# Kernel tuning notes

Hardware: AMD Instinct MI355X
Metric: run time of the kernel (lower is better)

## Reference

```python
import jax, jax.numpy as jnp
import numpy as np

N = 50000      # nodes
E = 400000     # edges
IN = 256       # in_dim
OUT = 64       # out_dim per head
ED = 64        # edge_dim
H = 4          # num_heads


def setup_inputs() -> dict:
    key = jax.random.key(0)
    ks = jax.random.split(key, 12)
    s = 0.05  # weight scale
    return {
        "x": jax.random.normal(ks[0], (N, IN), jnp.float32),
        "edge_index": jax.random.randint(ks[1], (2, E), 0, N),
        "edge_attr": jax.random.normal(ks[2], (E, ED), jnp.float32),
        # per-head stacked parameters
        "W_fc": jax.random.normal(ks[3], (H, IN, OUT), jnp.float32) * s,
        "b_fc": jnp.zeros((H, OUT), jnp.float32),
        "W_att": jax.random.normal(ks[4], (H, 2 * OUT + ED), jnp.float32) * s,
        "b_att": jnp.zeros((H,), jnp.float32),
        "W_edge": jax.random.normal(ks[5], (H, ED, OUT), jnp.float32) * s,
        "b_edge": jnp.zeros((H, OUT), jnp.float32),
        "W_eatt": jax.random.normal(ks[6], (H, ED, ED), jnp.float32) * s,
        "b_eatt": jnp.zeros((H, ED), jnp.float32),
    }


def reference(x, edge_index, edge_attr, W_fc, b_fc, W_att, b_att,
              W_edge, b_edge, W_eatt, b_eatt):
    src = edge_index[0]  # x_j (source / message sender)
    dst = edge_index[1]  # x_i (destination / aggregation index)

    # node transform per head: z[h] = x @ W_fc[h] + b_fc[h]   -> [H, N, OUT]
    z = jnp.einsum('ni,hio->hno', x, W_fc) + b_fc[:, None, :]
    # edge transform for attention calc: [H, E, ED]
    ea = jnp.einsum('ef,hfg->heg', edge_attr, W_eatt) + b_eatt[:, None, :]
    # edge transform for aggregation: [H, E, OUT]
    ez = jnp.einsum('ef,hfo->heo', edge_attr, W_edge) + b_edge[:, None, :]

    # attn_fc(cat[x_i, x_j, ea]) decomposed: W_att = [Wi | Wj | We]
    Wi = W_att[:, :OUT]            # [H, OUT]
    Wj = W_att[:, OUT:2 * OUT]     # [H, OUT]
    We = W_att[:, 2 * OUT:]        # [H, ED]
    a_node_i = jnp.einsum('hno,ho->hn', z, Wi)  # [H, N]
    a_node_j = jnp.einsum('hno,ho->hn', z, Wj)  # [H, N]
    a = (a_node_i[:, dst] + a_node_j[:, src]
         + jnp.einsum('heg,hg->he', ea, We) + b_att[:, None])  # [H, E]
    e = jax.nn.leaky_relu(a, negative_slope=0.2)

    # segment softmax over destination nodes, per head
    seg_max = jax.vmap(lambda v: jax.ops.segment_max(v, dst, num_segments=N))(e)
    exp_e = jnp.exp(e - seg_max[:, dst])
    seg_sum = jax.vmap(lambda v: jax.ops.segment_sum(v, dst, num_segments=N))(exp_e)
    alpha = exp_e / seg_sum[:, dst]  # [H, E]

    # weighted message: alpha * (x_j + ez), scatter-add to destination
    msg = alpha[:, :, None] * (z[:, src, :] + ez)  # [H, E, OUT]
    out = jax.vmap(lambda m: jax.ops.segment_sum(m, dst, num_segments=N))(msg)  # [H, N, OUT]

    # merge == 'cat' over heads -> [N, H*OUT]
    cat_out = jnp.transpose(out, (1, 0, 2)).reshape(N, H * OUT)
    return cat_out, alpha
```

## Files before the change

### kernel.cpp

```cpp
#include <hip/hip_runtime.h>
#include <math.h>

#define N_NODES 50000
#define N_EDGES 400000
#define IN_F 256
#define OUT_F 64
#define ED_F 64
#define NH 4
#define SCAN_NB ((N_NODES + 255) / 256)

using f16x8 = __attribute__((ext_vector_type(8))) _Float16;
using f32x4 = __attribute__((ext_vector_type(4))) float;

__global__ __launch_bounds__(256) void prep_kernel(
    const float* __restrict__ W_att, const float* __restrict__ b_att,
    const float* __restrict__ W_eatt, const float* __restrict__ b_eatt,
    const float* __restrict__ W_fc, const float* __restrict__ W_edge,
    float* __restrict__ u, float* __restrict__ c,
    _Float16* __restrict__ Wfcfrag, _Float16* __restrict__ Wefrag)
{
    const int b = blockIdx.x, t = threadIdx.x;
    if (b == 0) {
        int h = t >> 6, f = t & 63;
        const float* We = W_att + h * (2 * OUT_F + ED_F) + 2 * OUT_F;
        float s = 0.f;
        for (int g = 0; g < ED_F; g++) s += W_eatt[(h * ED_F + f) * ED_F + g] * We[g];
        u[t] = s;
        if (f == 0) {
            float cc = b_att[h];
            for (int g = 0; g < ED_F; g++) cc += b_eatt[h * ED_F + g] * We[g];
            c[h] = cc;
        }
    } else if (b <= 32) {
        int idx = b - 1;
        int h = idx >> 3, kt = idx & 7;
        int lane = t & 63, nt = t >> 6;
        int q = lane >> 4, l15 = lane & 15;
        f16x8 w;
#pragma unroll
        for (int j = 0; j < 8; j++) {
            int k = kt * 32 + q * 8 + j;
            int o = nt * 16 + l15;
            w[j] = (_Float16)W_fc[((size_t)h * IN_F + k) * OUT_F + o];
        }
        *(f16x8*)&Wfcfrag[(size_t)(((h * 8 + kt) * 4 + nt) * 64 + lane) * 8] = w;
    } else {
        int idx = b - 33;
        int h = idx >> 1, kt = idx & 1;
        int lane = t & 63, nt = t >> 6;
        int q = lane >> 4, l15 = lane & 15;
        f16x8 w;
#pragma unroll
        for (int j = 0; j < 8; j++) {
            int k = kt * 32 + q * 8 + j;
            int o = nt * 16 + l15;
            w[j] = (_Float16)W_edge[((size_t)h * ED_F + k) * OUT_F + o];
        }
        *(f16x8*)&Wefrag[(size_t)(((h * 2 + kt) * 4 + nt) * 64 + lane) * 8] = w;
    }
}

__global__ __launch_bounds__(256) void z_gemm(
    const float* __restrict__ x, const _Float16* __restrict__ Wfcfrag,
    const float* __restrict__ b_fc, const float* __restrict__ W_att,
    _Float16* __restrict__ zb, float* __restrict__ a_i, float* __restrict__ a_j)
{
    __shared__ _Float16 aLDS[32 * 64 * 8];
    const int t = threadIdx.x;
    const int n0 = blockIdx.x * 64;
    const int lane = t & 63, h = t >> 6;
    const int q = lane >> 4, l15 = lane & 15;

    {
        const int m = t >> 2, qq = t & 3;
        const int n = n0 + m;
#pragma unroll
        for (int p = 0; p < 4; p++) {
            float4 v4[4];
            if (n < N_NODES) {
                const float4* xp = (const float4*)(x + (size_t)n * IN_F + p * 64 + qq * 16);
#pragma unroll
                for (int k = 0; k < 4; k++) v4[k] = xp[k];
            } else {
#pragma unroll
                for (int k = 0; k < 4; k++) v4[k] = make_float4(0.f, 0.f, 0.f, 0.f);
            }
            const float* vv = (const float*)v4;
#pragma unroll
            for (int i = 0; i < 2; i++) {
                int c8 = p * 8 + qq * 2 + i;
                f16x8 w;
#pragma unroll
                for (int j = 0; j < 8; j++) w[j] = (_Float16)vv[i * 8 + j];
                *(f16x8*)&aLDS[(c8 * 64 + m) * 8] = w;
            }
        }
    }
    __syncthreads();

    f32x4 acc[4][4];
#pragma unroll
    for (int mt = 0; mt < 4; mt++)
#pragma unroll
        for (int nt = 0; nt < 4; nt++) acc[mt][nt] = (f32x4)0.f;

    for (int kt = 0; kt < 8; kt++) {
        f16x8 bfr[4];
#pragma unroll
        for (int nt = 0; nt < 4; nt++)
            bfr[nt] = *(const f16x8*)&Wfcfrag[(size_t)(((h * 8 + kt) * 4 + nt) * 64 + lane) * 8];
        f16x8 afr[4];
#pragma unroll
        for (int mt = 0; mt < 4; mt++)
            afr[mt] = *(f16x8*)&aLDS[((kt * 4 + q) * 64 + mt * 16 + l15) * 8];
#pragma unroll
        for (int mt = 0; mt < 4; mt++)
#pragma unroll
            for (int nt = 0; nt < 4; nt++)
                acc[mt][nt] = __builtin_amdgcn_mfma_f32_16x16x32_f16(afr[mt], bfr[nt], acc[mt][nt], 0, 0, 0);
    }

    float bfc[4], wiv[4], wjv[4];
#pragma unroll
    for (int nt = 0; nt < 4; nt++) {
        bfc[nt] = b_fc[h * OUT_F + nt * 16 + l15];
        wiv[nt] = W_att[h * 192 + nt * 16 + l15];
        wjv[nt] = W_att[h * 192 + 64 + nt * 16 + l15];
    }

#pragma unroll
    for (int mt = 0; mt < 4; mt++) {
#pragma unroll
        for (int r = 0; r < 4; r++) {
            const int node = n0 + mt * 16 + q * 4 + r;
            float zv[4];
            float pi = 0.f, pj = 0.f;
#pragma unroll
            for (int nt = 0; nt < 4; nt++) {
                zv[nt] = acc[mt][nt][r] + bfc[nt];
                pi += zv[nt] * wiv[nt];
                pj += zv[nt] * wjv[nt];
            }
#pragma unroll
            for (int m = 8; m; m >>= 1) {
                pi += __shfl_xor(pi, m, 64);
                pj += __shfl_xor(pj, m, 64);
            }
            if (node < N_NODES) {
                _Float16* zrow = zb + ((size_t)h * N_NODES + node) * OUT_F;
#pragma unroll
                for (int nt = 0; nt < 4; nt++)
                    zrow[nt * 16 + l15] = (_Float16)zv[nt];
                if (l15 == 0) {
                    a_i[h * N_NODES + node] = pi;
                    a_j[h * N_NODES + node] = pj;
                }
            }
        }
    }
}


__global__ __launch_bounds__(256) void hist_kernel(
    const int* __restrict__ edge_index, int* __restrict__ deg)
{
    const int e = blockIdx.x * 256 + threadIdx.x;
    if (e < N_EDGES) atomicAdd(&deg[edge_index[N_EDGES + e]], 1);
}

__global__ __launch_bounds__(256) void scan1_kernel(
    const int* __restrict__ deg, int* __restrict__ row_ptr, int* __restrict__ bsum)
{
    __shared__ int wsum[4];
    const int t = threadIdx.x, lane = t & 63, w = t >> 6;
    const int idx = blockIdx.x * 256 + t;
    int v = (idx < N_NODES) ? deg[idx] : 0;
    int x = v;
#pragma unroll
    for (int off = 1; off < 64; off <<= 1) {
        int y = __shfl_up(x, off, 64);
        if (lane >= off) x += y;
    }
    if (lane == 63) wsum[w] = x;
    __syncthreads();
    int woff = 0;
#pragma unroll
    for (int i = 0; i < 4; i++) if (i < w) woff += wsum[i];
    if (idx < N_NODES) row_ptr[idx] = woff + x - v;
    if (t == 255) bsum[blockIdx.x] = woff + x;
}

__global__ __launch_bounds__(256) void scan2_kernel(int* __restrict__ bsum)
{
    __shared__ int wsum[4];
    const int t = threadIdx.x, lane = t & 63, w = t >> 6;
    int v = (t < SCAN_NB) ? bsum[t] : 0;
    int x = v;
#pragma unroll
    for (int off = 1; off < 64; off <<= 1) {
        int y = __shfl_up(x, off, 64);
        if (lane >= off) x += y;
    }
    if (lane == 63) wsum[w] = x;
    __syncthreads();
    int woff = 0;
#pragma unroll
    for (int i = 0; i < 4; i++) if (i < w) woff += wsum[i];
    __syncthreads();
    if (t < SCAN_NB) bsum[t] = woff + x - v;
}

__global__ __launch_bounds__(256) void scan3_kernel(
    const int* __restrict__ bsum, int* __restrict__ row_ptr, int* __restrict__ cursor)
{
    const int idx = blockIdx.x * 256 + threadIdx.x;
    if (idx < N_NODES) {
        int rp = row_ptr[idx] + bsum[blockIdx.x];
        row_ptr[idx] = rp;
        cursor[idx] = rp;
    } else if (idx == N_NODES) {
        row_ptr[N_NODES] = N_EDGES;
    }
}

__global__ __launch_bounds__(256) void scatter_kernel(
    const int* __restrict__ edge_index, int* __restrict__ cursor,
    int* __restrict__ eorig, int* __restrict__ ssrc, int* __restrict__ sdst)
{
    const int e = blockIdx.x * 256 + threadIdx.x;
    if (e >= N_EDGES) return;
    const int d = edge_index[N_EDGES + e];
    const int pos = atomicAdd(&cursor[d], 1);
    eorig[pos] = e;
    ssrc[pos] = edge_index[e];
    sdst[pos] = d;
}

__global__ __launch_bounds__(256) void logits_kernel(
    const int* __restrict__ ssrc, const int* __restrict__ sdst,
    const int* __restrict__ eorig, const float* __restrict__ edge_attr,
    const float* __restrict__ u, const float* __restrict__ c,
    const float* __restrict__ a_i, const float* __restrict__ a_j,
    float* __restrict__ eperm)
{
    __shared__ float uS[NH * ED_F];
    __shared__ float cS[NH];
    const int t = threadIdx.x;
    uS[t] = u[t];
    if (t < NH) cS[t] = c[t];
    __syncthreads();

    const int p = blockIdx.x * 256 + t;
    if (p >= N_EDGES) return;
    const int e = eorig[p];
    const int src = ssrc[p];
    const int dst = sdst[p];
    const float4* ap = (const float4*)(edge_attr + (size_t)e * ED_F);

    float acc[NH] = {0.f, 0.f, 0.f, 0.f};
#pragma unroll
    for (int j = 0; j < 16; j++) {
        const float4 v = ap[j];
#pragma unroll
        for (int h = 0; h < NH; h++) {
            const float4 uv = *(const float4*)&uS[h * ED_F + j * 4];
            acc[h] += v.x * uv.x + v.y * uv.y + v.z * uv.z + v.w * uv.w;
        }
    }
#pragma unroll
    for (int h = 0; h < NH; h++) {
        float a = acc[h] + a_i[h * N_NODES + dst] + a_j[h * N_NODES + src] + cS[h];
        float ev = a > 0.f ? a : 0.2f * a;
        eperm[(size_t)h * N_EDGES + p] = ev;
    }
}

__global__ __launch_bounds__(256) void softmax_kernel(
    const int* __restrict__ row_ptr, const int* __restrict__ eorig,
    float* __restrict__ eperm, float* __restrict__ alpha_out)
{
    const int n = blockIdx.x * 256 + threadIdx.x;
    if (n >= N_NODES) return;
    const int b = row_ptr[n], en = row_ptr[n + 1];
    if (b >= en) return;
    const int h = blockIdx.y;
    float* ep = eperm + (size_t)h * N_EDGES;
    float* ao = alpha_out + (size_t)h * N_EDGES;
    float m = -INFINITY;
    for (int p = b; p < en; p++) m = fmaxf(m, ep[p]);
    float s = 0.f;
    for (int p = b; p < en; p++) { float v = expf(ep[p] - m); ep[p] = v; s += v; }
    const float inv = 1.f / s;
    for (int p = b; p < en; p++) {
        float a = ep[p] * inv;
        ep[p] = a;
        ao[eorig[p]] = a;
    }
}

__global__ __launch_bounds__(256) void aggregate_mfma(
    const int* __restrict__ ssrc, const int* __restrict__ sdst,
    const int* __restrict__ eorig, const float* __restrict__ edge_attr,
    const _Float16* __restrict__ Wefrag, const float* __restrict__ b_edge,
    const _Float16* __restrict__ zb, const float* __restrict__ eperm,
    float* __restrict__ out)
{
    __shared__ float smem[NH * 32 * 66];
    __shared__ int srcS[64], dstS[64];
    __shared__ float alphaS[NH][64];
    _Float16* aLDS = (_Float16*)smem;

    const int t = threadIdx.x;
    const int p0 = blockIdx.x * 64;
    const int lane = t & 63, h = t >> 6;
    const int q = lane >> 4, l15 = lane & 15;

    if (t < 64) srcS[t] = ssrc[p0 + t];
    else if (t < 128) dstS[t - 64] = sdst[p0 + t - 64];

    {
        const int m = t >> 2, qq = t & 3;
        const int er = eorig[p0 + m];
        const float4* ap = (const float4*)(edge_attr + (size_t)er * ED_F + qq * 16);
        float4 v4[4];
#pragma unroll
        for (int k = 0; k < 4; k++) v4[k] = ap[k];
        const float* vv = (const float*)v4;
#pragma unroll
        for (int i = 0; i < 2; i++) {
            int c8 = qq * 2 + i;
            f16x8 w;
#pragma unroll
            for (int j = 0; j < 8; j++) w[j] = (_Float16)vv[i * 8 + j];
            *(f16x8*)&aLDS[(c8 * 64 + m) * 8] = w;
        }
    }

    alphaS[h][lane] = eperm[(size_t)h * N_EDGES + p0 + lane];

    __syncthreads();

    f16x8 wf[2][4];
#pragma unroll
    for (int kt = 0; kt < 2; kt++)
#pragma unroll
        for (int nt = 0; nt < 4; nt++)
            wf[kt][nt] = *(const f16x8*)&Wefrag[(size_t)(((h * 2 + kt) * 4 + nt) * 64 + lane) * 8];

    f32x4 acc[4][4];
#pragma unroll
    for (int mt = 0; mt < 4; mt++)
#pragma unroll
        for (int nt = 0; nt < 4; nt++) acc[mt][nt] = (f32x4)0.f;

#pragma unroll
    for (int kt = 0; kt < 2; kt++) {
        f16x8 afr[4];
#pragma unroll
        for (int mt = 0; mt < 4; mt++)
            afr[mt] = *(f16x8*)&aLDS[((kt * 4 + q) * 64 + mt * 16 + l15) * 8];
#pragma unroll
        for (int mt = 0; mt < 4; mt++)
#pragma unroll
            for (int nt = 0; nt < 4; nt++)
                acc[mt][nt] = __builtin_amdgcn_mfma_f32_16x16x32_f16(afr[mt], wf[kt][nt], acc[mt][nt], 0, 0, 0);
    }

    __syncthreads();

    const float beL = b_edge[h * OUT_F + lane];
    int cur = dstS[0];
    float accv = 0.f;

#pragma unroll
    for (int half = 0; half < 2; half++) {
#pragma unroll
        for (int mh = 0; mh < 2; mh++) {
            const int mt = half * 2 + mh;
#pragma unroll
            for (int r = 0; r < 4; r++) {
                const int elh = mh * 16 + q * 4 + r;
#pragma unroll
                for (int nt = 0; nt < 4; nt++)
                    smem[(h * 32 + elh) * 66 + nt * 16 + l15] = acc[mt][nt][r];
            }
        }
        __syncthreads();

        float zf[32];
#pragma unroll
        for (int i = 0; i < 32; i++)
            zf[i] = (float)zb[((size_t)h * N_NODES + srcS[half * 32 + i]) * OUT_F + lane];

#pragma unroll
        for (int i = 0; i < 32; i++) {
            const int el = half * 32 + i;
            const int d = dstS[el];
            const float msg = smem[(h * 32 + i) * 66 + lane];
            const float al = alphaS[h][el];
            if (d != cur) {
                atomicAdd(&out[(size_t)cur * (NH * OUT_F) + h * OUT_F + lane], accv);
                accv = 0.f;
                cur = d;
            }
            accv += al * (msg + beL + zf[i]);
        }
        __syncthreads();
    }
    atomicAdd(&out[(size_t)cur * (NH * OUT_F) + h * OUT_F + lane], accv);
}

extern "C" void kernel_launch(void* const* d_in, const int* in_sizes, int n_in,
                              void* d_out, int out_size, void* d_ws, size_t ws_size,
                              hipStream_t stream) {
    const float* x         = (const float*)d_in[0];
    const int*   edge_index= (const int*)  d_in[1];
    const float* edge_attr = (const float*)d_in[2];
    const float* W_fc      = (const float*)d_in[3];
    const float* b_fc      = (const float*)d_in[4];
    const float* W_att     = (const float*)d_in[5];
    const float* b_att     = (const float*)d_in[6];
    const float* W_edge    = (const float*)d_in[7];
    const float* b_edge    = (const float*)d_in[8];
    const float* W_eatt    = (const float*)d_in[9];
    const float* b_eatt    = (const float*)d_in[10];

    float* out  = (float*)d_out;
    float* ebuf = out + (size_t)N_NODES * NH * OUT_F;

    _Float16* zb   = (_Float16*)d_ws;
    float* a_i     = (float*)(zb + (size_t)NH * N_NODES * OUT_F);
    float* a_j     = a_i + NH * N_NODES;
    float* eperm   = a_j + NH * N_NODES;
    float* u       = eperm + (size_t)NH * N_EDGES;
    float* c       = u + NH * 64;
    int* deg       = (int*)(c + NH);
    int* cursor    = deg + N_NODES;
    int* row_ptr   = cursor + N_NODES;
    int* eorig     = row_ptr + (N_NODES + 16);
    int* ssrc      = eorig + N_EDGES;
    int* sdst      = ssrc + N_EDGES;
    int* bsum      = sdst + N_EDGES;
    _Float16* Wfcfrag = (_Float16*)(bsum + 256);
    _Float16* Wefrag  = Wfcfrag + NH * 8 * 4 * 64 * 8;
    size_t need = (size_t)((char*)(Wefrag + NH * 2 * 4 * 64 * 8) - (char*)d_ws);

    hipMemsetAsync(out, 0, (size_t)N_NODES * NH * OUT_F * sizeof(float), stream);

    if (ws_size < need) {
        hipMemsetAsync(ebuf, 0, (size_t)NH * N_EDGES * sizeof(float), stream);
        return;
    }

    hipMemsetAsync(deg, 0, N_NODES * sizeof(int), stream);

    prep_kernel<<<41, 256, 0, stream>>>(W_att, b_att, W_eatt, b_eatt, W_fc, W_edge,
                                        u, c, Wfcfrag, Wefrag);

    hist_kernel<<<(N_EDGES + 255) / 256, 256, 0, stream>>>(edge_index, deg);
    scan1_kernel<<<SCAN_NB, 256, 0, stream>>>(deg, row_ptr, bsum);
    scan2_kernel<<<1, 256, 0, stream>>>(bsum);
    scan3_kernel<<<SCAN_NB, 256, 0, stream>>>(bsum, row_ptr, cursor);
    scatter_kernel<<<(N_EDGES + 255) / 256, 256, 0, stream>>>(edge_index, cursor,
                                                              eorig, ssrc, sdst);

    z_gemm<<<(N_NODES + 63) / 64, 256, 0, stream>>>(x, Wfcfrag, b_fc, W_att,
                                                    zb, a_i, a_j);

    logits_kernel<<<(N_EDGES + 255) / 256, 256, 0, stream>>>(ssrc, sdst, eorig, edge_attr,
                                                             u, c, a_i, a_j, eperm);

    dim3 sg((N_NODES + 255) / 256, NH);
    softmax_kernel<<<sg, 256, 0, stream>>>(row_ptr, eorig, eperm, ebuf);

    aggregate_mfma<<<N_EDGES / 64, 256, 0, stream>>>(ssrc, sdst, eorig, edge_attr,
                                                     Wefrag, b_edge, zb, eperm, out);
}
```

Baseline: 441.8 us.

## Split softmax into per-node stats and recompute alpha in consumers

The per-node softmax kernel no longer writes normalized values back or scatters alpha. It only computes the row max and inverse sum per node and head. A new edge-parallel kernel writes alpha in original edge order with coalesced stores via an epos map, and the aggregation kernel recomputes alpha from the logits and those stats. The scatter kernel is also split so that ssrc/sdst are filled coalesced by a separate gather kernel, and the aggregation LDS staging is reworked to 16-row tiles without intermediate barriers. This adds extra kernel launches and recomputed exponentials in exchange for removing serial per-node writes and scattered stores.

```diff
diff --git a/kernel.cpp b/kernel.cpp
--- a/kernel.cpp
+++ b/kernel.cpp
@@ -225,15 +225,25 @@
 
 __global__ __launch_bounds__(256) void scatter_kernel(
     const int* __restrict__ edge_index, int* __restrict__ cursor,
-    int* __restrict__ eorig, int* __restrict__ ssrc, int* __restrict__ sdst)
+    int* __restrict__ eorig, int* __restrict__ epos)
 {
     const int e = blockIdx.x * 256 + threadIdx.x;
     if (e >= N_EDGES) return;
     const int d = edge_index[N_EDGES + e];
     const int pos = atomicAdd(&cursor[d], 1);
     eorig[pos] = e;
-    ssrc[pos] = edge_index[e];
-    sdst[pos] = d;
+    epos[e] = pos;
+}
+
+__global__ __launch_bounds__(256) void fill_kernel(
+    const int* __restrict__ edge_index, const int* __restrict__ eorig,
+    int* __restrict__ ssrc, int* __restrict__ sdst)
+{
+    const int p = blockIdx.x * 256 + threadIdx.x;
+    if (p >= N_EDGES) return;
+    const int e = eorig[p];
+    ssrc[p] = edge_index[e];
+    sdst[p] = edge_index[N_EDGES + e];
 }
 
 __global__ __launch_bounds__(256) void logits_kernel(
@@ -275,26 +285,38 @@
     }
 }
 
-__global__ __launch_bounds__(256) void softmax_kernel(
-    const int* __restrict__ row_ptr, const int* __restrict__ eorig,
-    float* __restrict__ eperm, float* __restrict__ alpha_out)
+__global__ __launch_bounds__(256) void stats_kernel(
+    const int* __restrict__ row_ptr, const float* __restrict__ eperm,
+    float* __restrict__ rmax, float* __restrict__ rinv)
 {
     const int n = blockIdx.x * 256 + threadIdx.x;
     if (n >= N_NODES) return;
     const int b = row_ptr[n], en = row_ptr[n + 1];
     if (b >= en) return;
     const int h = blockIdx.y;
-    float* ep = eperm + (size_t)h * N_EDGES;
-    float* ao = alpha_out + (size_t)h * N_EDGES;
+    const float* ep = eperm + (size_t)h * N_EDGES;
     float m = -INFINITY;
     for (int p = b; p < en; p++) m = fmaxf(m, ep[p]);
     float s = 0.f;
-    for (int p = b; p < en; p++) { float v = expf(ep[p] - m); ep[p] = v; s += v; }
-    const float inv = 1.f / s;
-    for (int p = b; p < en; p++) {
-        float a = ep[p] * inv;
-        ep[p] = a;
-        ao[eorig[p]] = a;
+    for (int p = b; p < en; p++) s += __expf(ep[p] - m);
+    rmax[h * N_NODES + n] = m;
+    rinv[h * N_NODES + n] = 1.f / s;
+}
+
+__global__ __launch_bounds__(256) void alpha_orig_kernel(
+    const int* __restrict__ edge_index, const int* __restrict__ epos,
+    const float* __restrict__ eperm, const float* __restrict__ rmax,
+    const float* __restrict__ rinv, float* __restrict__ ebuf)
+{
+    const int e = blockIdx.x * 256 + threadIdx.x;
+    if (e >= N_EDGES) return;
+    const int pos = epos[e];
+    const int dst = edge_index[N_EDGES + e];
+#pragma unroll
+    for (int h = 0; h < NH; h++) {
+        const float lg = eperm[(size_t)h * N_EDGES + pos];
+        ebuf[(size_t)h * N_EDGES + e] =
+            __expf(lg - rmax[h * N_NODES + dst]) * rinv[h * N_NODES + dst];
     }
 }
 
@@ -303,12 +325,13 @@
     const int* __restrict__ eorig, const float* __restrict__ edge_attr,
     const _Float16* __restrict__ Wefrag, const float* __restrict__ b_edge,
     const _Float16* __restrict__ zb, const float* __restrict__ eperm,
+    const float* __restrict__ rmax, const float* __restrict__ rinv,
     float* __restrict__ out)
 {
-    __shared__ float smem[NH * 32 * 66];
+    __shared__ float tbuf[NH * 16 * 66];
     __shared__ int srcS[64], dstS[64];
     __shared__ float alphaS[NH][64];
-    _Float16* aLDS = (_Float16*)smem;
+    _Float16* aLDS = (_Float16*)tbuf;
 
     const int t = threadIdx.x;
     const int p0 = blockIdx.x * 64;
@@ -335,10 +358,13 @@
             *(f16x8*)&aLDS[(c8 * 64 + m) * 8] = w;
         }
     }
-
-    alphaS[h][lane] = eperm[(size_t)h * N_EDGES + p0 + lane];
-
-    __syncthreads();
+    __syncthreads();
+
+    {
+        const int d = dstS[lane];
+        const float lg = eperm[(size_t)h * N_EDGES + p0 + lane];
+        alphaS[h][lane] = __expf(lg - rmax[h * N_NODES + d]) * rinv[h * N_NODES + d];
+    }
 
     f16x8 wf[2][4];
 #pragma unroll
@@ -373,39 +399,30 @@
     float accv = 0.f;
 
 #pragma unroll
-    for (int half = 0; half < 2; half++) {
-#pragma unroll
-        for (int mh = 0; mh < 2; mh++) {
-            const int mt = half * 2 + mh;
-#pragma unroll
-            for (int r = 0; r < 4; r++) {
-                const int elh = mh * 16 + q * 4 + r;
-#pragma unroll
-                for (int nt = 0; nt < 4; nt++)
-                    smem[(h * 32 + elh) * 66 + nt * 16 + l15] = acc[mt][nt][r];
-            }
-        }
-        __syncthreads();
-
-        float zf[32];
-#pragma unroll
-        for (int i = 0; i < 32; i++)
-            zf[i] = (float)zb[((size_t)h * N_NODES + srcS[half * 32 + i]) * OUT_F + lane];
-
-#pragma unroll
-        for (int i = 0; i < 32; i++) {
-            const int el = half * 32 + i;
+    for (int mt = 0; mt < 4; mt++) {
+#pragma unroll
+        for (int r = 0; r < 4; r++)
+#pragma unroll
+            for (int nt = 0; nt < 4; nt++)
+                tbuf[(h * 16 + q * 4 + r) * 66 + nt * 16 + l15] = acc[mt][nt][r];
+
+        float zf[16];
+#pragma unroll
+        for (int i = 0; i < 16; i++)
+            zf[i] = (float)zb[((size_t)h * N_NODES + srcS[mt * 16 + i]) * OUT_F + lane];
+
+#pragma unroll
+        for (int i = 0; i < 16; i++) {
+            const int el = mt * 16 + i;
             const int d = dstS[el];
-            const float msg = smem[(h * 32 + i) * 66 + lane];
-            const float al = alphaS[h][el];
+            const float msg = tbuf[(h * 16 + i) * 66 + lane];
             if (d != cur) {
                 atomicAdd(&out[(size_t)cur * (NH * OUT_F) + h * OUT_F + lane], accv);
                 accv = 0.f;
                 cur = d;
             }
-            accv += al * (msg + beL + zf[i]);
-        }
-        __syncthreads();
+            accv += alphaS[h][el] * (msg + beL + zf[i]);
+        }
     }
     atomicAdd(&out[(size_t)cur * (NH * OUT_F) + h * OUT_F + lane], accv);
 }
@@ -431,13 +448,16 @@
     _Float16* zb   = (_Float16*)d_ws;
     float* a_i     = (float*)(zb + (size_t)NH * N_NODES * OUT_F);
     float* a_j     = a_i + NH * N_NODES;
-    float* eperm   = a_j + NH * N_NODES;
+    float* rmax    = a_j + NH * N_NODES;
+    float* rinv    = rmax + NH * N_NODES;
+    float* eperm   = rinv + NH * N_NODES;
     float* u       = eperm + (size_t)NH * N_EDGES;
     float* c       = u + NH * 64;
     int* deg       = (int*)(c + NH);
     int* cursor    = deg + N_NODES;
     int* row_ptr   = cursor + N_NODES;
-    int* eorig     = row_ptr + (N_NODES + 16);
+    int* epos      = row_ptr + (N_NODES + 16);
+    int* eorig     = epos + N_EDGES;
     int* ssrc      = eorig + N_EDGES;
     int* sdst      = ssrc + N_EDGES;
     int* bsum      = sdst + N_EDGES;
@@ -462,7 +482,9 @@
     scan2_kernel<<<1, 256, 0, stream>>>(bsum);
     scan3_kernel<<<SCAN_NB, 256, 0, stream>>>(bsum, row_ptr, cursor);
     scatter_kernel<<<(N_EDGES + 255) / 256, 256, 0, stream>>>(edge_index, cursor,
-                                                              eorig, ssrc, sdst);
+                                                              eorig, epos);
+    fill_kernel<<<(N_EDGES + 255) / 256, 256, 0, stream>>>(edge_index, eorig,
+                                                           ssrc, sdst);
 
     z_gemm<<<(N_NODES + 63) / 64, 256, 0, stream>>>(x, Wfcfrag, b_fc, W_att,
                                                     zb, a_i, a_j);
@@ -470,9 +492,13 @@
     logits_kernel<<<(N_EDGES + 255) / 256, 256, 0, stream>>>(ssrc, sdst, eorig, edge_attr,
                                                              u, c, a_i, a_j, eperm);
 
-    dim3 sg((N_NODES + 255) / 256, NH);
-    softmax_kernel<<<sg, 256, 0, stream>>>(row_ptr, eorig, eperm, ebuf);
+    dim3 sg(SCAN_NB, NH);
+    stats_kernel<<<sg, 256, 0, stream>>>(row_ptr, eperm, rmax, rinv);
+
+    alpha_orig_kernel<<<(N_EDGES + 255) / 256, 256, 0, stream>>>(edge_index, epos,
+                                                                 eperm, rmax, rinv, ebuf);
 
     aggregate_mfma<<<N_EDGES / 64, 256, 0, stream>>>(ssrc, sdst, eorig, edge_attr,
-                                                     Wefrag, b_edge, zb, eperm, out);
-}
+                                                     Wefrag, b_edge, zb, eperm,
+                                                     rmax, rinv, out);
+}
```

After: 446.6 us. Within noise of the previous version (+1.1%).
